# Optimization experiments

Hardware: AMD Instinct MI355X
Metric: run time of the kernel (lower is better)

The kernel has to match this reference:

```python
import jax, jax.numpy as jnp
import numpy as np

N = 1024      # n_nodes
S = 32        # state_dim
M = 32        # message_dim
STEPS = 5     # n_steps


def setup_inputs() -> dict:
    key = jax.random.key(0)
    ks = jax.random.split(key, 12)
    w = lambda k, shape: jax.random.normal(k, shape, jnp.float32) * 0.02
    return {
        "J": jax.random.normal(ks[0], (N, N), jnp.float32),
        "b": jax.random.normal(ks[1], (N,), jnp.float32),
        # message_passing MLP (Linear(2S+3->M), Linear(M->M), Linear(M->M))
        "W1": w(ks[2], (M, 2 * S + 3)), "b1": jnp.zeros((M,), jnp.float32),
        "W2": w(ks[3], (M, M)),         "b2": jnp.zeros((M,), jnp.float32),
        "W3": w(ks[4], (M, M)),         "b3": jnp.zeros((M,), jnp.float32),
        # GRU(input=S+M, hidden=S). h0 is always zero in the original forward,
        # so weight_hh never contributes (only bias_hh does) and is omitted.
        "W_ih": w(ks[5], (3 * S, S + M)),
        "b_ih": w(ks[6], (3 * S,)),
        "b_hh": w(ks[7], (3 * S,)),
        # readout MLP (Linear(S->M), Linear(M->M), Linear(M->2))
        "R1": w(ks[8], (M, S)),  "rb1": jnp.zeros((M,), jnp.float32),
        "R2": w(ks[9], (M, M)),  "rb2": jnp.zeros((M,), jnp.float32),
        "R3": w(ks[10], (2, M)), "rb3": jnp.zeros((2,), jnp.float32),
    }


def reference(J, b, W1, b1, W2, b2, W3, b3, W_ih, b_ih, b_hh, R1, rb1, R2, rb2, R3, rb3):
    # Split first linear over the concat [h_i, h_j, J_ij, b_i, b_j] so the
    # [N, N, 2S+3] concat tensor is never materialized.
    W1a, W1b = W1[:, :S], W1[:, S:2 * S]
    wJ, wbi, wbj = W1[:, 2 * S], W1[:, 2 * S + 1], W1[:, 2 * S + 2]

    def step(h, _):
        hi = h @ W1a.T                       # [N, M] (sender part)
        hj = h @ W1b.T                       # [N, M] (receiver part)
        pre = (hi[:, None, :] + hj[None, :, :]
               + J[:, :, None] * wJ
               + b[:, None, None] * wbi
               + b[None, :, None] * wbj
               + b1)                          # [N, N, M]
        x = jax.nn.relu(pre)
        x = jax.nn.relu(x @ W2.T + b2)
        x = jax.nn.relu(x @ W3.T + b3)       # message_i_j: [N, N, M]
        m = x.sum(0)                          # message to node j: sum over senders i
        # GRU with zero initial hidden state: h' = (1-z) * n_gate
        gi = jnp.concatenate([h, m], axis=-1) @ W_ih.T + b_ih  # [N, 3S]
        r = jax.nn.sigmoid(gi[:, :S] + b_hh[:S])
        z = jax.nn.sigmoid(gi[:, S:2 * S] + b_hh[S:2 * S])
        n = jnp.tanh(gi[:, 2 * S:] + r * b_hh[2 * S:])
        return (1.0 - z) * n, None

    h0 = jnp.zeros((N, S), J.dtype)
    h, _ = jax.lax.scan(step, h0, None, length=STEPS)

    r = jax.nn.relu(h @ R1.T + rb1)
    r = jax.nn.relu(r @ R2.T + rb2)
    r = jax.nn.relu(r @ R3.T + rb3)          # [N, 2]
    return jax.nn.sigmoid(r)
```

## Files before the change

### kernel.cpp

```cpp
#include <hip/hip_runtime.h>
#include <math.h>

#define NN 1024

typedef __attribute__((ext_vector_type(8))) short bf16x8;
typedef __attribute__((ext_vector_type(4))) short bf16x4;
typedef __attribute__((ext_vector_type(4))) float f32x4;
typedef __attribute__((ext_vector_type(2))) float f32x2;
typedef __attribute__((ext_vector_type(4))) unsigned int u32x4;

#if __has_builtin(__builtin_amdgcn_mfma_f32_16x16x16bf16_1k)
#define HAVE_MFMA16 1
#define MFMA16(a, b, c) __builtin_amdgcn_mfma_f32_16x16x16bf16_1k((a), (b), (c), 0, 0, 0)
#else
#define HAVE_MFMA16 0
#endif

__device__ __forceinline__ float sigmoidf_(float x) { return 1.0f / (1.0f + __expf(-x)); }

__device__ __forceinline__ unsigned int pk2(float a, float b) {
    return __builtin_amdgcn_perm(__float_as_uint(a) + 0x8000u,
                                 __float_as_uint(b) + 0x8000u, 0x03020706u);
}
__device__ __forceinline__ unsigned int pkcvt(float a, float b) {
#if __has_builtin(__builtin_amdgcn_cvt_pk_bf16_f32)
    return __builtin_bit_cast(unsigned int, __builtin_amdgcn_cvt_pk_bf16_f32(a, b));
#else
    return pk2(a, b);
#endif
}
__device__ __forceinline__ unsigned short f2bf_rne(float a) {
    unsigned int ua = __float_as_uint(a);
    ua += 0x7fffu + ((ua >> 16) & 1u);
    return (unsigned short)(ua >> 16);
}
__device__ __forceinline__ unsigned int pk2b(float a, float b) {
    return (unsigned int)f2bf_rne(a) | ((unsigned int)f2bf_rne(b) << 16);
}

#define CFG_FLOATS 3584

__global__ __launch_bounds__(256) void k_pre(
    const float* __restrict__ J, const float* __restrict__ b,
    const float* __restrict__ W1, const float* __restrict__ b1,
    const float* __restrict__ W2, const float* __restrict__ b2,
    const float* __restrict__ W3, const float* __restrict__ b3,
    float* __restrict__ Jt, float* __restrict__ h,
    float* __restrict__ u0, float* __restrict__ v, float* __restrict__ cfg)
{
    __shared__ float tile[32][33];
    const int t = blockIdx.x;
    const int tid = threadIdx.x;
    if (t < 1024) {
        int tx = (t & 31) * 32, ty = (t >> 5) * 32;
        int x = tid & 31, y = tid >> 5;
#pragma unroll
        for (int r = 0; r < 4; r++)
            tile[y + 8 * r][x] = J[(size_t)(ty + y + 8 * r) * NN + tx + x];
        __syncthreads();
#pragma unroll
        for (int r = 0; r < 4; r++)
            Jt[(size_t)(tx + y + 8 * r) * NN + ty + x] = tile[x][y + 8 * r];
    } else if (t < 1152) {
        int idx = (t - 1024) * 256 + tid;
        int row = idx >> 5, mm = idx & 31;
        float bi = b[row];
        h[idx]  = 0.f;
        u0[idx] = bi * W1[mm * 67 + 65];
        v[idx]  = fmaf(bi, W1[mm * 67 + 66], b1[mm]);
    } else if (tid < 64) {
        const int l = tid, p = l & 15, q = l >> 4;
        union FU { unsigned int d[4]; unsigned short s[8]; } t0, t1, t2, t3;
        float wj[8];
#pragma unroll
        for (int jj = 0; jj < 8; jj++) {
            int k = q * 8 + jj;
            t0.s[jj] = f2bf_rne(W2[p * 32 + k]);
            t1.s[jj] = f2bf_rne(W2[(16 + p) * 32 + k]);
            t2.s[jj] = f2bf_rne(W3[p * 32 + k]);
            t3.s[jj] = f2bf_rne(W3[(16 + p) * 32 + k]);
            wj[jj] = W1[k * 67 + 64];
        }
        u32x4* cw = (u32x4*)cfg;
        cw[l]       = *(u32x4*)t0.d;
        cw[64 + l]  = *(u32x4*)t1.d;
        cw[128 + l] = *(u32x4*)t2.d;
        cw[192 + l] = *(u32x4*)t3.d;
        f32x4* cf = (f32x4*)(cfg + 1024);
        f32x4 v0, v1, v2, v3;
#pragma unroll
        for (int r = 0; r < 4; r++) {
            v0[r] = b2[q * 4 + r];  v1[r] = b2[16 + q * 4 + r];
            v2[r] = b3[q * 4 + r];  v3[r] = b3[16 + q * 4 + r];
        }
        cf[l] = v0; cf[64 + l] = v1; cf[128 + l] = v2; cf[192 + l] = v3;
        f32x4* cj = (f32x4*)(cfg + 2048);
        f32x4 wlo, whi;
#pragma unroll
        for (int r = 0; r < 4; r++) { wlo[r] = wj[r]; whi[r] = wj[4 + r]; }
        cj[l] = wlo; cj[64 + l] = whi;

        const int g = p;
        u32x4 fa, fb;
        fa[0] = pk2b(W3[g * 32 + 4 * q + 0],      W3[g * 32 + 4 * q + 1]);
        fa[1] = pk2b(W3[g * 32 + 4 * q + 2],      W3[g * 32 + 4 * q + 3]);
        fa[2] = pk2b(W3[g * 32 + 16 + 4 * q + 0], W3[g * 32 + 16 + 4 * q + 1]);
        fa[3] = pk2b(W3[g * 32 + 16 + 4 * q + 2], W3[g * 32 + 16 + 4 * q + 3]);
        fb[0] = pk2b(W3[(16 + g) * 32 + 4 * q + 0],      W3[(16 + g) * 32 + 4 * q + 1]);
        fb[1] = pk2b(W3[(16 + g) * 32 + 4 * q + 2],      W3[(16 + g) * 32 + 4 * q + 3]);
        fb[2] = pk2b(W3[(16 + g) * 32 + 16 + 4 * q + 0], W3[(16 + g) * 32 + 16 + 4 * q + 1]);
        fb[3] = pk2b(W3[(16 + g) * 32 + 16 + 4 * q + 2], W3[(16 + g) * 32 + 16 + 4 * q + 3]);
        u32x4* cw2 = (u32x4*)(cfg + 2560);
        cw2[l] = fa; cw2[64 + l] = fb;
        f32x4* cb3 = (f32x4*)(cfg + 3072);
        f32x4 r0, r1;
#pragma unroll
        for (int r = 0; r < 4; r++) { r0[r] = b3[g]; r1[r] = b3[16 + g]; }
        cb3[l] = r0; cb3[64 + l] = r1;
    }
}

__global__ __launch_bounds__(256, 4) void k_step(
    const float* __restrict__ Jt, const float* __restrict__ cfg,
    const float* __restrict__ Wih, const float* __restrict__ bih,
    const float* __restrict__ bhh, const float* __restrict__ b,
    const float* __restrict__ b1, const float* __restrict__ W1,
    const float* __restrict__ R1, const float* __restrict__ rb1,
    const float* __restrict__ R2, const float* __restrict__ rb2,
    const float* __restrict__ R3, const float* __restrict__ rb3,
    float* __restrict__ h, float* __restrict__ v,
    const float* __restrict__ ui, float* __restrict__ uo,
    float* __restrict__ out, int do_out)
{
    __shared__ float red[4 * 32];
    __shared__ float hm[64], gbuf[96], hnb[32], tb[32];

    const int tid = threadIdx.x;
    const int w = tid >> 6;
    const int l = tid & 63;
    const int p = l & 15;
    const int q = l >> 4;
    const int j = blockIdx.x;

    union FU { bf16x8 v; u32x4 u4; } w2a0, w2a1;
    const u32x4* cw = (const u32x4*)cfg;
    w2a0.u4 = cw[l]; w2a1.u4 = cw[64 + l];
    const f32x4* cf = (const f32x4*)(cfg + 1024);
    const f32x4 b2v0 = cf[l], b2v1 = cf[64 + l];
    const f32x4* cj = (const f32x4*)(cfg + 2048);
    const f32x4 wlo = cj[l], whi = cj[64 + l];
    f32x2 wj2[4] = { {wlo[0], wlo[1]}, {wlo[2], wlo[3]}, {whi[0], whi[1]}, {whi[2], whi[3]} };

#if HAVE_MFMA16
    union B4 { bf16x4 v; unsigned int d[2]; } B0a, B1a, B0b, B1b;
    {
        const u32x4* cw2 = (const u32x4*)(cfg + 2560);
        u32x4 fa = cw2[l], fb = cw2[64 + l];
        B0a.d[0] = fa[0]; B0a.d[1] = fa[1]; B1a.d[0] = fa[2]; B1a.d[1] = fa[3];
        B0b.d[0] = fb[0]; B0b.d[1] = fb[1]; B1b.d[0] = fb[2]; B1b.d[1] = fb[3];
    }
    const f32x4* cb3 = (const f32x4*)(cfg + 3072);
    const f32x4 b3lo = cb3[l], b3hi = cb3[64 + l];
#else
    union FU w3a0, w3a1;
    w3a0.u4 = cw[128 + l]; w3a1.u4 = cw[192 + l];
    const f32x4 b3v0 = cf[128 + l], b3v1 = cf[192 + l];
    const int s0 = (p | ((l & 16) << 1)) << 2;
    const int s1 = s0 + 64;
    const bool qlo = (l & 32) == 0;
#endif

    f32x2 vv2[4];
    {
        float4 va = *(const float4*)(v + j * 32 + q * 8);
        float4 vb = *(const float4*)(v + j * 32 + q * 8 + 4);
        vv2[0] = f32x2{va.x, va.y}; vv2[1] = f32x2{va.z, va.w};
        vv2[2] = f32x2{vb.x, vb.y}; vv2[3] = f32x2{vb.z, vb.w};
    }

    f32x4 acc0 = {0.f, 0.f, 0.f, 0.f}, acc1 = {0.f, 0.f, 0.f, 0.f};

    const int ibase = w * 256;
    const float* jp = Jt + (size_t)j * NN + ibase + p;
    const float* up = ui + (size_t)(ibase + p) * 32 + q * 8;

    float  jw0[2], jw1[2];
    float4 ua0[2], ub0[2], ua1[2], ub1[2];
#pragma unroll
    for (int s = 0; s < 2; s++) {
        jw0[s] = jp[s * 32];       jw1[s] = jp[s * 32 + 16];
        ua0[s] = *(const float4*)(up + (size_t)s * 1024);
        ub0[s] = *(const float4*)(up + (size_t)s * 1024 + 4);
        ua1[s] = *(const float4*)(up + (size_t)s * 1024 + 512);
        ub1[s] = *(const float4*)(up + (size_t)s * 1024 + 516);
    }

#pragma unroll
    for (int tt = 0; tt < 8; ++tt) {
        const int sl = tt & 1;
        const float  jwA_c = jw0[sl], jwB_c = jw1[sl];
        const float4 uaA_c = ua0[sl], ubA_c = ub0[sl];
        const float4 uaB_c = ua1[sl], ubB_c = ub1[sl];
        if (tt < 6) {
            const float* jn = jp + (tt + 2) * 32;
            const float* un = up + (size_t)(tt + 2) * 1024;
            jw0[sl] = jn[0];  jw1[sl] = jn[16];
            ua0[sl] = *(const float4*)(un);
            ub0[sl] = *(const float4*)(un + 4);
            ua1[sl] = *(const float4*)(un + 512);
            ub1[sl] = *(const float4*)(un + 516);
        }

#pragma unroll
        for (int half = 0; half < 2; ++half) {
            const float  jw = half ? jwB_c : jwA_c;
            const float4 ua_c = half ? uaB_c : uaA_c;
            const float4 ub_c = half ? ubB_c : ubA_c;

            const f32x2 jw2 = {jw, jw};
            const f32x2 z2 = {0.f, 0.f};
            const f32x4 z4 = {0.f, 0.f, 0.f, 0.f};

            f32x2 x0 = {ua_c.x, ua_c.y}, x1 = {ua_c.z, ua_c.w};
            f32x2 x2 = {ub_c.x, ub_c.y}, x3 = {ub_c.z, ub_c.w};
            x0 = jw2 * wj2[0] + (x0 + vv2[0]);
            x1 = jw2 * wj2[1] + (x1 + vv2[1]);
            x2 = jw2 * wj2[2] + (x2 + vv2[2]);
            x3 = jw2 * wj2[3] + (x3 + vv2[3]);
            x0 = __builtin_elementwise_max(x0, z2);
            x1 = __builtin_elementwise_max(x1, z2);
            x2 = __builtin_elementwise_max(x2, z2);
            x3 = __builtin_elementwise_max(x3, z2);

            union BU { u32x4 u4; bf16x8 v; unsigned int d[4]; } bx;
            bx.d[0] = pkcvt(x0[0], x0[1]);
            bx.d[1] = pkcvt(x1[0], x1[1]);
            bx.d[2] = pkcvt(x2[0], x2[1]);
            bx.d[3] = pkcvt(x3[0], x3[1]);

            f32x4 c0 = __builtin_amdgcn_mfma_f32_16x16x32_bf16(w2a0.v, bx.v, b2v0, 0, 0, 0);
            f32x4 c1 = __builtin_amdgcn_mfma_f32_16x16x32_bf16(w2a1.v, bx.v, b2v1, 0, 0, 0);
            c0 = __builtin_elementwise_max(c0, z4);
            c1 = __builtin_elementwise_max(c1, z4);

#if HAVE_MFMA16
            union B4 { bf16x4 v; unsigned int d[2]; } A0, A1;
            A0.d[0] = pkcvt(c0[0], c0[1]); A0.d[1] = pkcvt(c0[2], c0[3]);
            A1.d[0] = pkcvt(c1[0], c1[1]); A1.d[1] = pkcvt(c1[2], c1[3]);

            f32x4 e0 = MFMA16(A0.v, B0a.v, b3lo);
            e0 = MFMA16(A1.v, B1a.v, e0);
            f32x4 e1 = MFMA16(A0.v, B0b.v, b3hi);
            e1 = MFMA16(A1.v, B1b.v, e1);
            acc0 = acc0 + __builtin_elementwise_max(e0, z4);
            acc1 = acc1 + __builtin_elementwise_max(e1, z4);
#else
            const int d0 = (int)pkcvt(c0[0], c0[1]);
            const int d1 = (int)pkcvt(c0[2], c0[3]);
            const int d2 = (int)pkcvt(c1[0], c1[1]);
            const int d3 = (int)pkcvt(c1[2], c1[3]);
            const int A0_ = __builtin_amdgcn_ds_bpermute(s0, d0);
            const int A1_ = __builtin_amdgcn_ds_bpermute(s0, d1);
            const int A2_ = __builtin_amdgcn_ds_bpermute(s1, d0);
            const int A3_ = __builtin_amdgcn_ds_bpermute(s1, d1);
            const int B0_ = __builtin_amdgcn_ds_bpermute(s0, d2);
            const int B1_ = __builtin_amdgcn_ds_bpermute(s0, d3);
            const int B2_ = __builtin_amdgcn_ds_bpermute(s1, d2);
            const int B3_ = __builtin_amdgcn_ds_bpermute(s1, d3);
            union BU yr;
            yr.d[0] = (unsigned)(qlo ? A0_ : B0_);
            yr.d[1] = (unsigned)(qlo ? A1_ : B1_);
            yr.d[2] = (unsigned)(qlo ? A2_ : B2_);
            yr.d[3] = (unsigned)(qlo ? A3_ : B3_);
            f32x4 e0 = __builtin_amdgcn_mfma_f32_16x16x32_bf16(w3a0.v, yr.v, b3v0, 0, 0, 0);
            f32x4 e1 = __builtin_amdgcn_mfma_f32_16x16x32_bf16(w3a1.v, yr.v, b3v1, 0, 0, 0);
            acc0 = acc0 + __builtin_elementwise_max(e0, z4);
            acc1 = acc1 + __builtin_elementwise_max(e1, z4);
#endif
        }
    }

#if HAVE_MFMA16
    float s0v = acc0[0] + acc0[1] + acc0[2] + acc0[3];
    float s1v = acc1[0] + acc1[1] + acc1[2] + acc1[3];
    s0v += __shfl_xor(s0v, 16);  s0v += __shfl_xor(s0v, 32);
    s1v += __shfl_xor(s1v, 16);  s1v += __shfl_xor(s1v, 32);
    if (l < 16) { red[w * 32 + l] = s0v;  red[w * 32 + 16 + l] = s1v; }
#else
#pragma unroll
    for (int bit = 1; bit < 16; bit <<= 1) {
#pragma unroll
        for (int r = 0; r < 4; r++) {
            acc0[r] += __shfl_xor(acc0[r], bit);
            acc1[r] += __shfl_xor(acc1[r], bit);
        }
    }
    if (p == 0) {
#pragma unroll
        for (int r = 0; r < 4; r++) {
            red[w * 32 + q * 4 + r]      = acc0[r];
            red[w * 32 + 16 + q * 4 + r] = acc1[r];
        }
    }
#endif
    __syncthreads();

    if (tid < 64) {
        float val;
        if (tid < 32) val = h[j * 32 + tid];
        else {
            int s = tid - 32;
            val = red[s] + red[32 + s] + red[64 + s] + red[96 + s];
        }
        hm[tid] = val;
    }
    __syncthreads();

    if (tid < 192) {
        const int row = tid >> 1, half = tid & 1;
        const float* wr = Wih + row * 64 + half * 32;
        const float* hh = hm + half * 32;
        float acc = 0.f;
#pragma unroll
        for (int k4 = 0; k4 < 8; k4++) {
            float4 w4 = *(const float4*)(wr + 4 * k4);
            acc = fmaf(w4.x, hh[4 * k4 + 0], acc);
            acc = fmaf(w4.y, hh[4 * k4 + 1], acc);
            acc = fmaf(w4.z, hh[4 * k4 + 2], acc);
            acc = fmaf(w4.w, hh[4 * k4 + 3], acc);
        }
        acc += __shfl_xor(acc, 1);
        if (half == 0) gbuf[row] = acc + bih[row];
    }
    __syncthreads();

    if (tid < 32) {
        const int s = tid;
        float r = sigmoidf_(gbuf[s] + bhh[s]);
        float z = sigmoidf_(gbuf[32 + s] + bhh[32 + s]);
        float n = tanhf(gbuf[64 + s] + r * bhh[64 + s]);
        float hn_ = (1.0f - z) * n;
        hnb[s] = hn_;
        h[j * 32 + s] = hn_;
    }
    __syncthreads();

    if (tid < 64) {
        const int s = tid & 31;
        const bool isV = tid >= 32;
        const float bj = b[j];
        const float* wr = W1 + s * 67 + (isV ? 32 : 0);
        float acc = isV ? fmaf(bj, W1[s * 67 + 66], b1[s]) : bj * W1[s * 67 + 65];
#pragma unroll
        for (int k = 0; k < 32; k++) acc = fmaf(wr[k], hnb[k], acc);
        if (isV) v[j * 32 + s] = acc;
        else     uo[j * 32 + s] = acc;
    }

    if (do_out) {
        __syncthreads();
        if (tid < 32) {
            float a = rb1[tid];
            const float* rr = R1 + tid * 32;
#pragma unroll 8
            for (int k = 0; k < 32; k++) a = fmaf(rr[k], hnb[k], a);
            gbuf[tid] = fmaxf(a, 0.f);
        }
        __syncthreads();
        if (tid < 32) {
            float a = rb2[tid];
            const float* rr = R2 + tid * 32;
#pragma unroll 8
            for (int k = 0; k < 32; k++) a = fmaf(rr[k], gbuf[k], a);
            tb[tid] = fmaxf(a, 0.f);
        }
        __syncthreads();
        if (tid < 2) {
            float a = rb3[tid];
            const float* rr = R3 + tid * 32;
#pragma unroll 8
            for (int k = 0; k < 32; k++) a = fmaf(rr[k], tb[k], a);
            out[j * 2 + tid] = sigmoidf_(fmaxf(a, 0.f));
        }
    }
}

extern "C" void kernel_launch(void* const* d_in, const int* in_sizes, int n_in,
                              void* d_out, int out_size, void* d_ws, size_t ws_size,
                              hipStream_t stream)
{
    const float* J   = (const float*)d_in[0];
    const float* b   = (const float*)d_in[1];
    const float* W1  = (const float*)d_in[2];
    const float* b1  = (const float*)d_in[3];
    const float* W2  = (const float*)d_in[4];
    const float* b2  = (const float*)d_in[5];
    const float* W3  = (const float*)d_in[6];
    const float* b3  = (const float*)d_in[7];
    const float* Wih = (const float*)d_in[8];
    const float* bih = (const float*)d_in[9];
    const float* bhh = (const float*)d_in[10];
    const float* R1  = (const float*)d_in[11];
    const float* rb1 = (const float*)d_in[12];
    const float* R2  = (const float*)d_in[13];
    const float* rb2 = (const float*)d_in[14];
    const float* R3  = (const float*)d_in[15];
    const float* rb3 = (const float*)d_in[16];

    float* out = (float*)d_out;
    float* ws  = (float*)d_ws;
    float* h   = ws;
    float* v   = ws + 32768;
    float* u0  = ws + 65536;
    float* u1  = ws + 98304;
    float* Jt  = ws + 131072;
    float* cfg = ws + 131072 + NN * NN;

    k_pre<<<1153, 256, 0, stream>>>(J, b, W1, b1, W2, b2, W3, b3,
                                    Jt, h, u0, v, cfg);
    for (int s = 0; s < 5; s++) {
        const float* ui = (s & 1) ? u1 : u0;
        float*       uo = (s & 1) ? u0 : u1;
        k_step<<<1024, 256, 0, stream>>>(Jt, cfg, Wih, bih, bhh, b, b1, W1,
                                         R1, rb1, R2, rb2, R3, rb3,
                                         h, v, ui, uo, out, (s == 4) ? 1 : 0);
    }
}
```

Measured before the change: 199.8 us.

## Remove pre-kernel: gather J column into LDS per step and specialize first step

Drops the separate preprocessing kernel that transposed J and packed weight fragments. Each step block now gathers its J column directly from global memory into shared memory with strided loads, and converts W2/W3 to bf16 fragments in registers. A templated first-step variant computes u and v from b directly, since h is zero on that step, and no longer reads workspace. This removes one launch and the full transpose pass over J. The cost is uncoalesced column reads of J in every step and repeated per-block weight conversion.

Measured after the change: 226.9 us. +13.6%, slower.

```diff
diff --git a/kernel.cpp b/kernel.cpp
--- a/kernel.cpp
+++ b/kernel.cpp
@@ -38,93 +38,14 @@
     return (unsigned int)f2bf_rne(a) | ((unsigned int)f2bf_rne(b) << 16);
 }
 
-#define CFG_FLOATS 3584
-
-__global__ __launch_bounds__(256) void k_pre(
+template<int S0>
+__global__ __launch_bounds__(256, 4) void k_step(
     const float* __restrict__ J, const float* __restrict__ b,
     const float* __restrict__ W1, const float* __restrict__ b1,
     const float* __restrict__ W2, const float* __restrict__ b2,
     const float* __restrict__ W3, const float* __restrict__ b3,
-    float* __restrict__ Jt, float* __restrict__ h,
-    float* __restrict__ u0, float* __restrict__ v, float* __restrict__ cfg)
-{
-    __shared__ float tile[32][33];
-    const int t = blockIdx.x;
-    const int tid = threadIdx.x;
-    if (t < 1024) {
-        int tx = (t & 31) * 32, ty = (t >> 5) * 32;
-        int x = tid & 31, y = tid >> 5;
-#pragma unroll
-        for (int r = 0; r < 4; r++)
-            tile[y + 8 * r][x] = J[(size_t)(ty + y + 8 * r) * NN + tx + x];
-        __syncthreads();
-#pragma unroll
-        for (int r = 0; r < 4; r++)
-            Jt[(size_t)(tx + y + 8 * r) * NN + ty + x] = tile[x][y + 8 * r];
-    } else if (t < 1152) {
-        int idx = (t - 1024) * 256 + tid;
-        int row = idx >> 5, mm = idx & 31;
-        float bi = b[row];
-        h[idx]  = 0.f;
-        u0[idx] = bi * W1[mm * 67 + 65];
-        v[idx]  = fmaf(bi, W1[mm * 67 + 66], b1[mm]);
-    } else if (tid < 64) {
-        const int l = tid, p = l & 15, q = l >> 4;
-        union FU { unsigned int d[4]; unsigned short s[8]; } t0, t1, t2, t3;
-        float wj[8];
-#pragma unroll
-        for (int jj = 0; jj < 8; jj++) {
-            int k = q * 8 + jj;
-            t0.s[jj] = f2bf_rne(W2[p * 32 + k]);
-            t1.s[jj] = f2bf_rne(W2[(16 + p) * 32 + k]);
-            t2.s[jj] = f2bf_rne(W3[p * 32 + k]);
-            t3.s[jj] = f2bf_rne(W3[(16 + p) * 32 + k]);
-            wj[jj] = W1[k * 67 + 64];
-        }
-        u32x4* cw = (u32x4*)cfg;
-        cw[l]       = *(u32x4*)t0.d;
-        cw[64 + l]  = *(u32x4*)t1.d;
-        cw[128 + l] = *(u32x4*)t2.d;
-        cw[192 + l] = *(u32x4*)t3.d;
-        f32x4* cf = (f32x4*)(cfg + 1024);
-        f32x4 v0, v1, v2, v3;
-#pragma unroll
-        for (int r = 0; r < 4; r++) {
-            v0[r] = b2[q * 4 + r];  v1[r] = b2[16 + q * 4 + r];
-            v2[r] = b3[q * 4 + r];  v3[r] = b3[16 + q * 4 + r];
-        }
-        cf[l] = v0; cf[64 + l] = v1; cf[128 + l] = v2; cf[192 + l] = v3;
-        f32x4* cj = (f32x4*)(cfg + 2048);
-        f32x4 wlo, whi;
-#pragma unroll
-        for (int r = 0; r < 4; r++) { wlo[r] = wj[r]; whi[r] = wj[4 + r]; }
-        cj[l] = wlo; cj[64 + l] = whi;
-
-        const int g = p;
-        u32x4 fa, fb;
-        fa[0] = pk2b(W3[g * 32 + 4 * q + 0],      W3[g * 32 + 4 * q + 1]);
-        fa[1] = pk2b(W3[g * 32 + 4 * q + 2],      W3[g * 32 + 4 * q + 3]);
-        fa[2] = pk2b(W3[g * 32 + 16 + 4 * q + 0], W3[g * 32 + 16 + 4 * q + 1]);
-        fa[3] = pk2b(W3[g * 32 + 16 + 4 * q + 2], W3[g * 32 + 16 + 4 * q + 3]);
-        fb[0] = pk2b(W3[(16 + g) * 32 + 4 * q + 0],      W3[(16 + g) * 32 + 4 * q + 1]);
-        fb[1] = pk2b(W3[(16 + g) * 32 + 4 * q + 2],      W3[(16 + g) * 32 + 4 * q + 3]);
-        fb[2] = pk2b(W3[(16 + g) * 32 + 16 + 4 * q + 0], W3[(16 + g) * 32 + 16 + 4 * q + 1]);
-        fb[3] = pk2b(W3[(16 + g) * 32 + 16 + 4 * q + 2], W3[(16 + g) * 32 + 16 + 4 * q + 3]);
-        u32x4* cw2 = (u32x4*)(cfg + 2560);
-        cw2[l] = fa; cw2[64 + l] = fb;
-        f32x4* cb3 = (f32x4*)(cfg + 3072);
-        f32x4 r0, r1;
-#pragma unroll
-        for (int r = 0; r < 4; r++) { r0[r] = b3[g]; r1[r] = b3[16 + g]; }
-        cb3[l] = r0; cb3[64 + l] = r1;
-    }
-}
-
-__global__ __launch_bounds__(256, 4) void k_step(
-    const float* __restrict__ Jt, const float* __restrict__ cfg,
     const float* __restrict__ Wih, const float* __restrict__ bih,
-    const float* __restrict__ bhh, const float* __restrict__ b,
-    const float* __restrict__ b1, const float* __restrict__ W1,
+    const float* __restrict__ bhh,
     const float* __restrict__ R1, const float* __restrict__ rb1,
     const float* __restrict__ R2, const float* __restrict__ rb2,
     const float* __restrict__ R3, const float* __restrict__ rb3,
@@ -132,7 +53,9 @@
     const float* __restrict__ ui, float* __restrict__ uo,
     float* __restrict__ out, int do_out)
 {
-    __shared__ float red[4 * 32];
+    __shared__ float jcol[1024];
+    __shared__ float bcol[1024];
+    __shared__ float red[128];
     __shared__ float hm[64], gbuf[96], hnb[32], tb[32];
 
     const int tid = threadIdx.x;
@@ -142,36 +65,70 @@
     const int q = l >> 4;
     const int j = blockIdx.x;
 
-    union FU { bf16x8 v; u32x4 u4; } w2a0, w2a1;
-    const u32x4* cw = (const u32x4*)cfg;
-    w2a0.u4 = cw[l]; w2a1.u4 = cw[64 + l];
-    const f32x4* cf = (const f32x4*)(cfg + 1024);
-    const f32x4 b2v0 = cf[l], b2v1 = cf[64 + l];
-    const f32x4* cj = (const f32x4*)(cfg + 2048);
-    const f32x4 wlo = cj[l], whi = cj[64 + l];
-    f32x2 wj2[4] = { {wlo[0], wlo[1]}, {wlo[2], wlo[3]}, {whi[0], whi[1]}, {whi[2], whi[3]} };
+#pragma unroll
+    for (int k = 0; k < 4; k++)
+        jcol[k * 256 + tid] = J[(size_t)(k * 256 + tid) * NN + j];
+    if (S0) {
+#pragma unroll
+        for (int k = 0; k < 4; k++)
+            bcol[k * 256 + tid] = b[k * 256 + tid];
+    }
+
+    union FU { bf16x8 v; u32x4 u4; unsigned int d[4]; } w2a0, w2a1;
+#pragma unroll
+    for (int i = 0; i < 4; i++) {
+        w2a0.d[i] = pk2b(W2[p * 32 + q * 8 + 2 * i],        W2[p * 32 + q * 8 + 2 * i + 1]);
+        w2a1.d[i] = pk2b(W2[(16 + p) * 32 + q * 8 + 2 * i], W2[(16 + p) * 32 + q * 8 + 2 * i + 1]);
+    }
+    f32x4 b2v0, b2v1;
+#pragma unroll
+    for (int r = 0; r < 4; r++) { b2v0[r] = b2[q * 4 + r]; b2v1[r] = b2[16 + q * 4 + r]; }
+    f32x2 wj2[4], wbi2[4];
+#pragma unroll
+    for (int i = 0; i < 4; i++) {
+        wj2[i] = f32x2{W1[(q * 8 + 2 * i) * 67 + 64], W1[(q * 8 + 2 * i + 1) * 67 + 64]};
+        if (S0)
+            wbi2[i] = f32x2{W1[(q * 8 + 2 * i) * 67 + 65], W1[(q * 8 + 2 * i + 1) * 67 + 65]};
+    }
 
 #if HAVE_MFMA16
     union B4 { bf16x4 v; unsigned int d[2]; } B0a, B1a, B0b, B1b;
-    {
-        const u32x4* cw2 = (const u32x4*)(cfg + 2560);
-        u32x4 fa = cw2[l], fb = cw2[64 + l];
-        B0a.d[0] = fa[0]; B0a.d[1] = fa[1]; B1a.d[0] = fa[2]; B1a.d[1] = fa[3];
-        B0b.d[0] = fb[0]; B0b.d[1] = fb[1]; B1b.d[0] = fb[2]; B1b.d[1] = fb[3];
-    }
-    const f32x4* cb3 = (const f32x4*)(cfg + 3072);
-    const f32x4 b3lo = cb3[l], b3hi = cb3[64 + l];
+    B0a.d[0] = pk2b(W3[p * 32 + 4 * q + 0],      W3[p * 32 + 4 * q + 1]);
+    B0a.d[1] = pk2b(W3[p * 32 + 4 * q + 2],      W3[p * 32 + 4 * q + 3]);
+    B1a.d[0] = pk2b(W3[p * 32 + 16 + 4 * q + 0], W3[p * 32 + 16 + 4 * q + 1]);
+    B1a.d[1] = pk2b(W3[p * 32 + 16 + 4 * q + 2], W3[p * 32 + 16 + 4 * q + 3]);
+    B0b.d[0] = pk2b(W3[(16 + p) * 32 + 4 * q + 0],      W3[(16 + p) * 32 + 4 * q + 1]);
+    B0b.d[1] = pk2b(W3[(16 + p) * 32 + 4 * q + 2],      W3[(16 + p) * 32 + 4 * q + 3]);
+    B1b.d[0] = pk2b(W3[(16 + p) * 32 + 16 + 4 * q + 0], W3[(16 + p) * 32 + 16 + 4 * q + 1]);
+    B1b.d[1] = pk2b(W3[(16 + p) * 32 + 16 + 4 * q + 2], W3[(16 + p) * 32 + 16 + 4 * q + 3]);
+    f32x4 b3lo, b3hi;
+#pragma unroll
+    for (int r = 0; r < 4; r++) { b3lo[r] = b3[p]; b3hi[r] = b3[16 + p]; }
 #else
     union FU w3a0, w3a1;
-    w3a0.u4 = cw[128 + l]; w3a1.u4 = cw[192 + l];
-    const f32x4 b3v0 = cf[128 + l], b3v1 = cf[192 + l];
+#pragma unroll
+    for (int i = 0; i < 4; i++) {
+        w3a0.d[i] = pk2b(W3[p * 32 + q * 8 + 2 * i],        W3[p * 32 + q * 8 + 2 * i + 1]);
+        w3a1.d[i] = pk2b(W3[(16 + p) * 32 + q * 8 + 2 * i], W3[(16 + p) * 32 + q * 8 + 2 * i + 1]);
+    }
+    f32x4 b3v0, b3v1;
+#pragma unroll
+    for (int r = 0; r < 4; r++) { b3v0[r] = b3[q * 4 + r]; b3v1[r] = b3[16 + q * 4 + r]; }
     const int s0 = (p | ((l & 16) << 1)) << 2;
     const int s1 = s0 + 64;
     const bool qlo = (l & 32) == 0;
 #endif
 
     f32x2 vv2[4];
-    {
+    if (S0) {
+        const float bj = b[j];
+#pragma unroll
+        for (int i = 0; i < 4; i++) {
+            int m0 = q * 8 + 2 * i;
+            vv2[i] = f32x2{fmaf(bj, W1[m0 * 67 + 66], b1[m0]),
+                           fmaf(bj, W1[(m0 + 1) * 67 + 66], b1[m0 + 1])};
+        }
+    } else {
         float4 va = *(const float4*)(v + j * 32 + q * 8);
         float4 vb = *(const float4*)(v + j * 32 + q * 8 + 4);
         vv2[0] = f32x2{va.x, va.y}; vv2[1] = f32x2{va.z, va.w};
@@ -179,113 +136,119 @@
     }
 
     f32x4 acc0 = {0.f, 0.f, 0.f, 0.f}, acc1 = {0.f, 0.f, 0.f, 0.f};
-
     const int ibase = w * 256;
-    const float* jp = Jt + (size_t)j * NN + ibase + p;
-    const float* up = ui + (size_t)(ibase + p) * 32 + q * 8;
-
-    float  jw0[2], jw1[2];
-    float4 ua0[2], ub0[2], ua1[2], ub1[2];
-#pragma unroll
-    for (int s = 0; s < 2; s++) {
-        jw0[s] = jp[s * 32];       jw1[s] = jp[s * 32 + 16];
-        ua0[s] = *(const float4*)(up + (size_t)s * 1024);
-        ub0[s] = *(const float4*)(up + (size_t)s * 1024 + 4);
-        ua1[s] = *(const float4*)(up + (size_t)s * 1024 + 512);
-        ub1[s] = *(const float4*)(up + (size_t)s * 1024 + 516);
-    }
-
-#pragma unroll
-    for (int tt = 0; tt < 8; ++tt) {
-        const int sl = tt & 1;
-        const float  jwA_c = jw0[sl], jwB_c = jw1[sl];
-        const float4 uaA_c = ua0[sl], ubA_c = ub0[sl];
-        const float4 uaB_c = ua1[sl], ubB_c = ub1[sl];
-        if (tt < 6) {
-            const float* jn = jp + (tt + 2) * 32;
-            const float* un = up + (size_t)(tt + 2) * 1024;
-            jw0[sl] = jn[0];  jw1[sl] = jn[16];
-            ua0[sl] = *(const float4*)(un);
-            ub0[sl] = *(const float4*)(un + 4);
-            ua1[sl] = *(const float4*)(un + 512);
-            ub1[sl] = *(const float4*)(un + 516);
-        }
-
-#pragma unroll
-        for (int half = 0; half < 2; ++half) {
-            const float  jw = half ? jwB_c : jwA_c;
-            const float4 ua_c = half ? uaB_c : uaA_c;
-            const float4 ub_c = half ? ubB_c : ubA_c;
-
-            const f32x2 jw2 = {jw, jw};
-            const f32x2 z2 = {0.f, 0.f};
-            const f32x4 z4 = {0.f, 0.f, 0.f, 0.f};
-
-            f32x2 x0 = {ua_c.x, ua_c.y}, x1 = {ua_c.z, ua_c.w};
-            f32x2 x2 = {ub_c.x, ub_c.y}, x3 = {ub_c.z, ub_c.w};
-            x0 = jw2 * wj2[0] + (x0 + vv2[0]);
-            x1 = jw2 * wj2[1] + (x1 + vv2[1]);
-            x2 = jw2 * wj2[2] + (x2 + vv2[2]);
-            x3 = jw2 * wj2[3] + (x3 + vv2[3]);
-            x0 = __builtin_elementwise_max(x0, z2);
-            x1 = __builtin_elementwise_max(x1, z2);
-            x2 = __builtin_elementwise_max(x2, z2);
-            x3 = __builtin_elementwise_max(x3, z2);
-
-            union BU { u32x4 u4; bf16x8 v; unsigned int d[4]; } bx;
-            bx.d[0] = pkcvt(x0[0], x0[1]);
-            bx.d[1] = pkcvt(x1[0], x1[1]);
-            bx.d[2] = pkcvt(x2[0], x2[1]);
-            bx.d[3] = pkcvt(x3[0], x3[1]);
-
-            f32x4 c0 = __builtin_amdgcn_mfma_f32_16x16x32_bf16(w2a0.v, bx.v, b2v0, 0, 0, 0);
-            f32x4 c1 = __builtin_amdgcn_mfma_f32_16x16x32_bf16(w2a1.v, bx.v, b2v1, 0, 0, 0);
-            c0 = __builtin_elementwise_max(c0, z4);
-            c1 = __builtin_elementwise_max(c1, z4);
+
+    auto do_half = [&](float jw, f32x2 s0v, f32x2 s1v, f32x2 s2v, f32x2 s3v) {
+        const f32x2 jw2v = {jw, jw};
+        const f32x2 z2 = {0.f, 0.f};
+        const f32x4 z4 = {0.f, 0.f, 0.f, 0.f};
+        f32x2 x0 = jw2v * wj2[0] + s0v;
+        f32x2 x1 = jw2v * wj2[1] + s1v;
+        f32x2 x2 = jw2v * wj2[2] + s2v;
+        f32x2 x3 = jw2v * wj2[3] + s3v;
+        x0 = __builtin_elementwise_max(x0, z2);
+        x1 = __builtin_elementwise_max(x1, z2);
+        x2 = __builtin_elementwise_max(x2, z2);
+        x3 = __builtin_elementwise_max(x3, z2);
+
+        union BU { u32x4 u4; bf16x8 v; unsigned int d[4]; } bx;
+        bx.d[0] = pkcvt(x0[0], x0[1]);
+        bx.d[1] = pkcvt(x1[0], x1[1]);
+        bx.d[2] = pkcvt(x2[0], x2[1]);
+        bx.d[3] = pkcvt(x3[0], x3[1]);
+
+        f32x4 c0 = __builtin_amdgcn_mfma_f32_16x16x32_bf16(w2a0.v, bx.v, b2v0, 0, 0, 0);
+        f32x4 c1 = __builtin_amdgcn_mfma_f32_16x16x32_bf16(w2a1.v, bx.v, b2v1, 0, 0, 0);
+        c0 = __builtin_elementwise_max(c0, z4);
+        c1 = __builtin_elementwise_max(c1, z4);
 
 #if HAVE_MFMA16
-            union B4 { bf16x4 v; unsigned int d[2]; } A0, A1;
-            A0.d[0] = pkcvt(c0[0], c0[1]); A0.d[1] = pkcvt(c0[2], c0[3]);
-            A1.d[0] = pkcvt(c1[0], c1[1]); A1.d[1] = pkcvt(c1[2], c1[3]);
-
-            f32x4 e0 = MFMA16(A0.v, B0a.v, b3lo);
-            e0 = MFMA16(A1.v, B1a.v, e0);
-            f32x4 e1 = MFMA16(A0.v, B0b.v, b3hi);
-            e1 = MFMA16(A1.v, B1b.v, e1);
-            acc0 = acc0 + __builtin_elementwise_max(e0, z4);
-            acc1 = acc1 + __builtin_elementwise_max(e1, z4);
-#else
-            const int d0 = (int)pkcvt(c0[0], c0[1]);
-            const int d1 = (int)pkcvt(c0[2], c0[3]);
-            const int d2 = (int)pkcvt(c1[0], c1[1]);
-            const int d3 = (int)pkcvt(c1[2], c1[3]);
-            const int A0_ = __builtin_amdgcn_ds_bpermute(s0, d0);
-            const int A1_ = __builtin_amdgcn_ds_bpermute(s0, d1);
-            const int A2_ = __builtin_amdgcn_ds_bpermute(s1, d0);
-            const int A3_ = __builtin_amdgcn_ds_bpermute(s1, d1);
-            const int B0_ = __builtin_amdgcn_ds_bpermute(s0, d2);
-            const int B1_ = __builtin_amdgcn_ds_bpermute(s0, d3);
-            const int B2_ = __builtin_amdgcn_ds_bpermute(s1, d2);
-            const int B3_ = __builtin_amdgcn_ds_bpermute(s1, d3);
-            union BU yr;
-            yr.d[0] = (unsigned)(qlo ? A0_ : B0_);
-            yr.d[1] = (unsigned)(qlo ? A1_ : B1_);
-            yr.d[2] = (unsigned)(qlo ? A2_ : B2_);
-            yr.d[3] = (unsigned)(qlo ? A3_ : B3_);
-            f32x4 e0 = __builtin_amdgcn_mfma_f32_16x16x32_bf16(w3a0.v, yr.v, b3v0, 0, 0, 0);
-            f32x4 e1 = __builtin_amdgcn_mfma_f32_16x16x32_bf16(w3a1.v, yr.v, b3v1, 0, 0, 0);
-            acc0 = acc0 + __builtin_elementwise_max(e0, z4);
-            acc1 = acc1 + __builtin_elementwise_max(e1, z4);
-#endif
+        union B4 { bf16x4 v; unsigned int d[2]; } A0, A1;
+        A0.d[0] = pkcvt(c0[0], c0[1]); A0.d[1] = pkcvt(c0[2], c0[3]);
+        A1.d[0] = pkcvt(c1[0], c1[1]); A1.d[1] = pkcvt(c1[2], c1[3]);
+
+        f32x4 e0 = MFMA16(A0.v, B0a.v, b3lo);
+        e0 = MFMA16(A1.v, B1a.v, e0);
+        f32x4 e1 = MFMA16(A0.v, B0b.v, b3hi);
+        e1 = MFMA16(A1.v, B1b.v, e1);
+        acc0 = acc0 + __builtin_elementwise_max(e0, z4);
+        acc1 = acc1 + __builtin_elementwise_max(e1, z4);
+#else
+        const int d0 = (int)pkcvt(c0[0], c0[1]);
+        const int d1 = (int)pkcvt(c0[2], c0[3]);
+        const int d2 = (int)pkcvt(c1[0], c1[1]);
+        const int d3 = (int)pkcvt(c1[2], c1[3]);
+        const int A0_ = __builtin_amdgcn_ds_bpermute(s0, d0);
+        const int A1_ = __builtin_amdgcn_ds_bpermute(s0, d1);
+        const int A2_ = __builtin_amdgcn_ds_bpermute(s1, d0);
+        const int A3_ = __builtin_amdgcn_ds_bpermute(s1, d1);
+        const int B0_ = __builtin_amdgcn_ds_bpermute(s0, d2);
+        const int B1_ = __builtin_amdgcn_ds_bpermute(s0, d3);
+        const int B2_ = __builtin_amdgcn_ds_bpermute(s1, d2);
+        const int B3_ = __builtin_amdgcn_ds_bpermute(s1, d3);
+        union BU yr;
+        yr.d[0] = (unsigned)(qlo ? A0_ : B0_);
+        yr.d[1] = (unsigned)(qlo ? A1_ : B1_);
+        yr.d[2] = (unsigned)(qlo ? A2_ : B2_);
+        yr.d[3] = (unsigned)(qlo ? A3_ : B3_);
+        f32x4 e0 = __builtin_amdgcn_mfma_f32_16x16x32_bf16(w3a0.v, yr.v, b3v0, 0, 0, 0);
+        f32x4 e1 = __builtin_amdgcn_mfma_f32_16x16x32_bf16(w3a1.v, yr.v, b3v1, 0, 0, 0);
+        acc0 = acc0 + __builtin_elementwise_max(e0, z4);
+        acc1 = acc1 + __builtin_elementwise_max(e1, z4);
+#endif
+    };
+
+    __syncthreads();
+
+    if (S0) {
+#pragma unroll
+        for (int tt = 0; tt < 8; ++tt) {
+            const int rb0 = ibase + p + 32 * tt;
+            const float jwA = jcol[rb0], jwB = jcol[rb0 + 16];
+            const float biA = bcol[rb0], biB = bcol[rb0 + 16];
+            const f32x2 bA = {biA, biA}, bB = {biB, biB};
+            do_half(jwA, bA * wbi2[0] + vv2[0], bA * wbi2[1] + vv2[1],
+                         bA * wbi2[2] + vv2[2], bA * wbi2[3] + vv2[3]);
+            do_half(jwB, bB * wbi2[0] + vv2[0], bB * wbi2[1] + vv2[1],
+                         bB * wbi2[2] + vv2[2], bB * wbi2[3] + vv2[3]);
+        }
+    } else {
+        const float* up = ui + (size_t)(ibase + p) * 32 + q * 8;
+        float4 ua0[2], ub0[2], ua1[2], ub1[2];
+#pragma unroll
+        for (int s = 0; s < 2; s++) {
+            ua0[s] = *(const float4*)(up + (size_t)s * 1024);
+            ub0[s] = *(const float4*)(up + (size_t)s * 1024 + 4);
+            ua1[s] = *(const float4*)(up + (size_t)s * 1024 + 512);
+            ub1[s] = *(const float4*)(up + (size_t)s * 1024 + 516);
+        }
+#pragma unroll
+        for (int tt = 0; tt < 8; ++tt) {
+            const int rb0 = ibase + p + 32 * tt;
+            const float jwA = jcol[rb0], jwB = jcol[rb0 + 16];
+            const int sl = tt & 1;
+            const float4 uaA = ua0[sl], ubA = ub0[sl];
+            const float4 uaB = ua1[sl], ubB = ub1[sl];
+            if (tt < 6) {
+                const float* un = up + (size_t)(tt + 2) * 1024;
+                ua0[sl] = *(const float4*)(un);
+                ub0[sl] = *(const float4*)(un + 4);
+                ua1[sl] = *(const float4*)(un + 512);
+                ub1[sl] = *(const float4*)(un + 516);
+            }
+            do_half(jwA, f32x2{uaA.x, uaA.y} + vv2[0], f32x2{uaA.z, uaA.w} + vv2[1],
+                         f32x2{ubA.x, ubA.y} + vv2[2], f32x2{ubA.z, ubA.w} + vv2[3]);
+            do_half(jwB, f32x2{uaB.x, uaB.y} + vv2[0], f32x2{uaB.z, uaB.w} + vv2[1],
+                         f32x2{ubB.x, ubB.y} + vv2[2], f32x2{ubB.z, ubB.w} + vv2[3]);
         }
     }
 
 #if HAVE_MFMA16
-    float s0v = acc0[0] + acc0[1] + acc0[2] + acc0[3];
-    float s1v = acc1[0] + acc1[1] + acc1[2] + acc1[3];
-    s0v += __shfl_xor(s0v, 16);  s0v += __shfl_xor(s0v, 32);
-    s1v += __shfl_xor(s1v, 16);  s1v += __shfl_xor(s1v, 32);
-    if (l < 16) { red[w * 32 + l] = s0v;  red[w * 32 + 16 + l] = s1v; }
+    float s0r = acc0[0] + acc0[1] + acc0[2] + acc0[3];
+    float s1r = acc1[0] + acc1[1] + acc1[2] + acc1[3];
+    s0r += __shfl_xor(s0r, 16);  s0r += __shfl_xor(s0r, 32);
+    s1r += __shfl_xor(s1r, 16);  s1r += __shfl_xor(s1r, 32);
+    if (l < 16) { red[w * 32 + l] = s0r;  red[w * 32 + 16 + l] = s1r; }
 #else
 #pragma unroll
     for (int bit = 1; bit < 16; bit <<= 1) {
@@ -307,10 +270,10 @@
 
     if (tid < 64) {
         float val;
-        if (tid < 32) val = h[j * 32 + tid];
+        if (tid < 32) val = S0 ? 0.f : h[j * 32 + tid];
         else {
-            int s = tid - 32;
-            val = red[s] + red[32 + s] + red[64 + s] + red[96 + s];
+            int ss = tid - 32;
+            val = red[ss] + red[32 + ss] + red[64 + ss] + red[96 + ss];
         }
         hm[tid] = val;
     }
@@ -335,26 +298,26 @@
     __syncthreads();
 
     if (tid < 32) {
-        const int s = tid;
-        float r = sigmoidf_(gbuf[s] + bhh[s]);
-        float z = sigmoidf_(gbuf[32 + s] + bhh[32 + s]);
-        float n = tanhf(gbuf[64 + s] + r * bhh[64 + s]);
+        const int ss = tid;
+        float r = sigmoidf_(gbuf[ss] + bhh[ss]);
+        float z = sigmoidf_(gbuf[32 + ss] + bhh[32 + ss]);
+        float n = tanhf(gbuf[64 + ss] + r * bhh[64 + ss]);
         float hn_ = (1.0f - z) * n;
-        hnb[s] = hn_;
-        h[j * 32 + s] = hn_;
+        hnb[ss] = hn_;
+        h[j * 32 + ss] = hn_;
     }
     __syncthreads();
 
     if (tid < 64) {
-        const int s = tid & 31;
+        const int ss = tid & 31;
         const bool isV = tid >= 32;
         const float bj = b[j];
-        const float* wr = W1 + s * 67 + (isV ? 32 : 0);
-        float acc = isV ? fmaf(bj, W1[s * 67 + 66], b1[s]) : bj * W1[s * 67 + 65];
+        const float* wr = W1 + ss * 67 + (isV ? 32 : 0);
+        float acc = isV ? fmaf(bj, W1[ss * 67 + 66], b1[ss]) : bj * W1[ss * 67 + 65];
 #pragma unroll
         for (int k = 0; k < 32; k++) acc = fmaf(wr[k], hnb[k], acc);
-        if (isV) v[j * 32 + s] = acc;
-        else     uo[j * 32 + s] = acc;
+        if (isV) v[j * 32 + ss] = acc;
+        else     uo[j * 32 + ss] = acc;
     }
 
     if (do_out) {
@@ -413,16 +376,19 @@
     float* v   = ws + 32768;
     float* u0  = ws + 65536;
     float* u1  = ws + 98304;
-    float* Jt  = ws + 131072;
-    float* cfg = ws + 131072 + NN * NN;
-
-    k_pre<<<1153, 256, 0, stream>>>(J, b, W1, b1, W2, b2, W3, b3,
-                                    Jt, h, u0, v, cfg);
+
     for (int s = 0; s < 5; s++) {
         const float* ui = (s & 1) ? u1 : u0;
         float*       uo = (s & 1) ? u0 : u1;
-        k_step<<<1024, 256, 0, stream>>>(Jt, cfg, Wih, bih, bhh, b, b1, W1,
-                                         R1, rb1, R2, rb2, R3, rb3,
-                                         h, v, ui, uo, out, (s == 4) ? 1 : 0);
-    }
-}
+        if (s == 0)
+            k_step<1><<<1024, 256, 0, stream>>>(J, b, W1, b1, W2, b2, W3, b3,
+                                                Wih, bih, bhh,
+                                                R1, rb1, R2, rb2, R3, rb3,
+                                                h, v, ui, uo, out, 0);
+        else
+            k_step<0><<<1024, 256, 0, stream>>>(J, b, W1, b1, W2, b2, W3, b3,
+                                                Wih, bih, bhh,
+                                                R1, rb1, R2, rb2, R3, rb3,
+                                                h, v, ui, uo, out, (s == 4) ? 1 : 0);
+    }
+}
```
